# Kernel tuning notes

Hardware: AMD Instinct MI355X
Metric: run time of the kernel (lower is better)

The kernel has to match this reference:

```python
import jax, jax.numpy as jnp
import numpy as np


def setup_inputs() -> dict:
    key = jax.random.key(0)
    k1, k2 = jax.random.split(key)
    L, B, C, H, W = 4, 8, 256, 64, 64
    inputs = jax.random.normal(k1, (L, B, C, H, W), dtype=jnp.float32)
    # nn.Linear(C, C, bias=False) weight: [out, in]
    Wlin = jax.random.normal(k2, (C, C), dtype=jnp.float32) * (1.0 / np.sqrt(C))
    return {"inputs": inputs, "W": Wlin}


def reference(inputs, W):
    # inputs: [L, B, C, H, W] -- stacked input_list; W: [C, C] linear weight
    # GAP over spatial dims -> [L, B, C]
    gap = jnp.mean(inputs, axis=(3, 4))
    # torch Linear: y = x @ W^T  -> scores [L, B, C]
    scores = jnp.einsum('lbc,dc->lbd', gap, W)
    # original loops over channels doing softmax over the layer axis;
    # vectorized: softmax across L for each (b, c)
    attn = jax.nn.softmax(scores, axis=0)  # [L, B, C]
    # broadcast multiply each level by its per-channel attention
    out = inputs * attn[:, :, :, None, None]
    return out
```

## Files before the change

kernel.cpp:

```cpp
#include <hip/hip_runtime.h>
#include <stdint.h>


#define L_DIM 4
#define B_DIM 8
#define C_DIM 256
#define HW    4096
#define F4_PER_CH (HW / 4)
#define NCH   (L_DIM * B_DIM * C_DIM)
#define NF4   ((size_t)NCH * F4_PER_CH)

__global__ __launch_bounds__(256) void gap_kernel(
        const float4* __restrict__ in, float* __restrict__ gap) {
    const int ch = blockIdx.x;
    const float4* base = in + (size_t)ch * F4_PER_CH;
    float s = 0.0f;
    #pragma unroll
    for (int k = 0; k < 4; ++k) {
        float4 p = base[threadIdx.x + k * 256];
        s += (p.x + p.y) + (p.z + p.w);
    }
    #pragma unroll
    for (int off = 32; off > 0; off >>= 1)
        s += __shfl_down(s, off, 64);
    __shared__ float wsum[4];
    const int wave = threadIdx.x >> 6;
    const int lane = threadIdx.x & 63;
    if (lane == 0) wsum[wave] = s;
    __syncthreads();
    if (threadIdx.x == 0) {
        float t = wsum[0] + wsum[1] + wsum[2] + wsum[3];
        gap[ch] = t * (1.0f / (float)HW);
    }
}

__global__ __launch_bounds__(256) void attn_kernel(
        const float* __restrict__ gap, const float* __restrict__ Wf,
        float* __restrict__ attn) {
    const int b = blockIdx.x;
    const int d = threadIdx.x;
    __shared__ float g[L_DIM][C_DIM];
    #pragma unroll
    for (int l = 0; l < L_DIM; ++l)
        g[l][d] = gap[(l * B_DIM + b) * C_DIM + d];
    __syncthreads();

    float acc[L_DIM] = {0.f, 0.f, 0.f, 0.f};
    const float* wrow = Wf + (size_t)d * C_DIM;
    #pragma unroll 4
    for (int c = 0; c < C_DIM; ++c) {
        float w = wrow[c];
        #pragma unroll
        for (int l = 0; l < L_DIM; ++l)
            acc[l] += g[l][c] * w;
    }
    float m = fmaxf(fmaxf(acc[0], acc[1]), fmaxf(acc[2], acc[3]));
    float e[L_DIM], se = 0.f;
    #pragma unroll
    for (int l = 0; l < L_DIM; ++l) { e[l] = __expf(acc[l] - m); se += e[l]; }
    float inv = 1.0f / se;
    #pragma unroll
    for (int l = 0; l < L_DIM; ++l)
        attn[(l * B_DIM + b) * C_DIM + d] = e[l] * inv;
}

__global__ __launch_bounds__(256) void scale_kernel(
        const float4* __restrict__ in, const float* __restrict__ attn,
        float4* __restrict__ out) {
    const size_t i = (size_t)blockIdx.x * 256 + threadIdx.x;
    float a = attn[i >> 10];
    float4 p = in[i];
    float4 q;
    q.x = p.x * a;
    q.y = p.y * a;
    q.z = p.z * a;
    q.w = p.w * a;
    out[i] = q;
}

extern "C" void kernel_launch(void* const* d_in, const int* in_sizes, int n_in,
                              void* d_out, int out_size, void* d_ws, size_t ws_size,
                              hipStream_t stream) {
    const float4* in_p  = (const float4*)d_in[0];
    const float*  W_p   = (const float*)d_in[1];
    float4*       out_p = (float4*)d_out;

    float* gap  = (float*)d_ws;
    float* attn = gap + NCH;

    gap_kernel<<<NCH, 256, 0, stream>>>(in_p, gap);
    attn_kernel<<<B_DIM, 256, 0, stream>>>(gap, W_p, attn);
    scale_kernel<<<(int)(NF4 / 256), 256, 0, stream>>>(in_p, attn, out_p);
}
```

Before: 254.7 us.

## Fuse attention matvec and softmax into the per-channel scale kernel

Removes the separate 8-block attention kernel, which was serial and under-occupied, and its launch. Each channel block of the scale pass now computes its own four dot products (one W row against the gap vectors of all levels), applies the softmax over levels, and scales its 4096 elements. Scale work moves from one element per thread to four per thread. The cost is redundant matvec work: each W row is reread across L*B blocks, plus two block barriers ahead of the streaming pass.

```diff
diff --git a/kernel.cpp b/kernel.cpp
--- a/kernel.cpp
+++ b/kernel.cpp
@@ -8,7 +8,6 @@
 #define HW    4096
 #define F4_PER_CH (HW / 4)
 #define NCH   (L_DIM * B_DIM * C_DIM)
-#define NF4   ((size_t)NCH * F4_PER_CH)
 
 __global__ __launch_bounds__(256) void gap_kernel(
         const float4* __restrict__ in, float* __restrict__ gap) {
@@ -29,53 +28,65 @@
     if (lane == 0) wsum[wave] = s;
     __syncthreads();
     if (threadIdx.x == 0) {
-        float t = wsum[0] + wsum[1] + wsum[2] + wsum[3];
-        gap[ch] = t * (1.0f / (float)HW);
+        gap[ch] = (wsum[0] + wsum[1] + wsum[2] + wsum[3]) * (1.0f / (float)HW);
     }
 }
 
-__global__ __launch_bounds__(256) void attn_kernel(
-        const float* __restrict__ gap, const float* __restrict__ Wf,
-        float* __restrict__ attn) {
-    const int b = blockIdx.x;
-    const int d = threadIdx.x;
-    __shared__ float g[L_DIM][C_DIM];
+__global__ __launch_bounds__(256) void attn_scale_kernel(
+        const float4* __restrict__ in, const float* __restrict__ gap,
+        const float* __restrict__ Wf, float4* __restrict__ out) {
+    const int ch = blockIdx.x;
+    const int d  = ch & (C_DIM - 1);
+    const int lb = ch >> 8;
+    const int b  = lb & (B_DIM - 1);
+    const int l  = lb >> 3;
+    const int c  = threadIdx.x;
+
+    const float w = Wf[(size_t)d * C_DIM + c];
+    float p0 = gap[(0 * B_DIM + b) * C_DIM + c] * w;
+    float p1 = gap[(1 * B_DIM + b) * C_DIM + c] * w;
+    float p2 = gap[(2 * B_DIM + b) * C_DIM + c] * w;
+    float p3 = gap[(3 * B_DIM + b) * C_DIM + c] * w;
+
     #pragma unroll
-    for (int l = 0; l < L_DIM; ++l)
-        g[l][d] = gap[(l * B_DIM + b) * C_DIM + d];
+    for (int off = 32; off > 0; off >>= 1) {
+        p0 += __shfl_down(p0, off, 64);
+        p1 += __shfl_down(p1, off, 64);
+        p2 += __shfl_down(p2, off, 64);
+        p3 += __shfl_down(p3, off, 64);
+    }
+    __shared__ float part[4][4];
+    __shared__ float a_bcast;
+    const int wave = threadIdx.x >> 6;
+    const int lane = threadIdx.x & 63;
+    if (lane == 0) {
+        part[wave][0] = p0; part[wave][1] = p1;
+        part[wave][2] = p2; part[wave][3] = p3;
+    }
     __syncthreads();
+    if (threadIdx.x == 0) {
+        float s0 = part[0][0] + part[1][0] + part[2][0] + part[3][0];
+        float s1 = part[0][1] + part[1][1] + part[2][1] + part[3][1];
+        float s2 = part[0][2] + part[1][2] + part[2][2] + part[3][2];
+        float s3 = part[0][3] + part[1][3] + part[2][3] + part[3][3];
+        float m  = fmaxf(fmaxf(s0, s1), fmaxf(s2, s3));
+        float e0 = __expf(s0 - m), e1 = __expf(s1 - m);
+        float e2 = __expf(s2 - m), e3 = __expf(s3 - m);
+        float el = (l == 0) ? e0 : (l == 1) ? e1 : (l == 2) ? e2 : e3;
+        a_bcast = el / (e0 + e1 + e2 + e3);
+    }
+    __syncthreads();
+    const float a = a_bcast;
 
-    float acc[L_DIM] = {0.f, 0.f, 0.f, 0.f};
-    const float* wrow = Wf + (size_t)d * C_DIM;
-    #pragma unroll 4
-    for (int c = 0; c < C_DIM; ++c) {
-        float w = wrow[c];
-        #pragma unroll
-        for (int l = 0; l < L_DIM; ++l)
-            acc[l] += g[l][c] * w;
+    const float4* src = in  + (size_t)ch * F4_PER_CH;
+    float4*       dst = out + (size_t)ch * F4_PER_CH;
+    #pragma unroll
+    for (int k = 0; k < 4; ++k) {
+        float4 p = src[threadIdx.x + k * 256];
+        float4 q;
+        q.x = p.x * a; q.y = p.y * a; q.z = p.z * a; q.w = p.w * a;
+        dst[threadIdx.x + k * 256] = q;
     }
-    float m = fmaxf(fmaxf(acc[0], acc[1]), fmaxf(acc[2], acc[3]));
-    float e[L_DIM], se = 0.f;
-    #pragma unroll
-    for (int l = 0; l < L_DIM; ++l) { e[l] = __expf(acc[l] - m); se += e[l]; }
-    float inv = 1.0f / se;
-    #pragma unroll
-    for (int l = 0; l < L_DIM; ++l)
-        attn[(l * B_DIM + b) * C_DIM + d] = e[l] * inv;
-}
-
-__global__ __launch_bounds__(256) void scale_kernel(
-        const float4* __restrict__ in, const float* __restrict__ attn,
-        float4* __restrict__ out) {
-    const size_t i = (size_t)blockIdx.x * 256 + threadIdx.x;
-    float a = attn[i >> 10];
-    float4 p = in[i];
-    float4 q;
-    q.x = p.x * a;
-    q.y = p.y * a;
-    q.z = p.z * a;
-    q.w = p.w * a;
-    out[i] = q;
 }
 
 extern "C" void kernel_launch(void* const* d_in, const int* in_sizes, int n_in,
@@ -85,10 +96,8 @@
     const float*  W_p   = (const float*)d_in[1];
     float4*       out_p = (float4*)d_out;
 
-    float* gap  = (float*)d_ws;
-    float* attn = gap + NCH;
+    float* gap = (float*)d_ws;
 
     gap_kernel<<<NCH, 256, 0, stream>>>(in_p, gap);
-    attn_kernel<<<B_DIM, 256, 0, stream>>>(gap, W_p, attn);
-    scale_kernel<<<(int)(NF4 / 256), 256, 0, stream>>>(in_p, attn, out_p);
+    attn_scale_kernel<<<NCH, 256, 0, stream>>>(in_p, gap, W_p, out_p);
 }
```

Result: faster. 244.1 us (-4.2%).
